# Kernel tuning notes

Measured on AMD Instinct MI355X. Metric: run time of the kernel, lower is better.

The kernel has to match this reference:

```python
import jax, jax.numpy as jnp
import numpy as np

B, S, D = 4, 256, 2048
E, F, K = 32, 768, 8


def setup_inputs() -> dict:
    key = jax.random.key(0)
    k1, k2, k3, k4, k5 = jax.random.split(key, 5)
    sc_in = 1.0 / np.sqrt(D)
    sc_f = 1.0 / np.sqrt(F)
    return {
        "hidden_states": jax.random.normal(k1, (B, S, D), jnp.float32),
        "gate_w": jax.random.normal(k2, (E, D), jnp.float32) * sc_in,   # nn.Linear(D, E).weight
        "wg": jax.random.normal(k3, (E, F, D), jnp.float32) * sc_in,    # gate_proj weights [E, F, D]
        "wu": jax.random.normal(k4, (E, F, D), jnp.float32) * sc_in,    # up_proj weights   [E, F, D]
        "wd": jax.random.normal(k5, (E, D, F), jnp.float32) * sc_f,     # down_proj weights [E, D, F]
    }


def reference(hidden_states, gate_w, wg, wu, wd):
    b, s, d = hidden_states.shape
    x = hidden_states.reshape(-1, d)                        # [T, D]
    T = x.shape[0]

    # Router: linear -> softmax over experts -> top-k -> renormalize
    router_logits = jnp.einsum("td,ed->te", x, gate_w)      # [T, E]
    routing_probs = jax.nn.softmax(router_logits, axis=-1)
    topk_w, topk_idx = jax.lax.top_k(routing_probs, K)      # [T, K]
    topk_w = topk_w / jnp.sum(topk_w, axis=-1, keepdims=True)  # norm_topk_prob=True

    # Scatter top-k weights to dense [T, E] combine weights (zeros for unselected experts)
    combine = jnp.zeros((T, wg.shape[0]), x.dtype).at[
        jnp.arange(T)[:, None], topk_idx
    ].set(topk_w)                                           # [T, E]

    # Expert gated MLPs (computed for all experts, combined with sparse weights)
    g = jnp.einsum("td,efd->etf", x, wg)                    # [E, T, F]
    u = jnp.einsum("td,efd->etf", x, wu)                    # [E, T, F]
    h = jax.nn.silu(g) * u                                  # [E, T, F]
    y = jnp.einsum("etf,edf->etd", h, wd)                   # [E, T, D]

    out = jnp.einsum("te,etd->td", combine, y)              # [T, D]
    return out.reshape(b, s, d)
```

## Files before the change

### kernel.cpp

```cpp
#include <hip/hip_runtime.h>

#define T_TOK 1024
#define D_DIM 2048
#define E_NUM 32
#define F_DIM 768
#define K_TOP 8

typedef __bf16 v8bf __attribute__((ext_vector_type(8)));
typedef float v4f __attribute__((ext_vector_type(4)));
typedef unsigned short v8us __attribute__((ext_vector_type(8)));

__device__ __forceinline__ unsigned short f2b(float f) {
  unsigned int u = __builtin_bit_cast(unsigned int, f);
  u += 0x7fffu + ((u >> 16) & 1u);
  return (unsigned short)(u >> 16);
}
__device__ __forceinline__ float b2f(unsigned short s) {
  return __builtin_bit_cast(float, (unsigned int)s << 16);
}
__device__ __forceinline__ v8us cvt8u(v4f a, v4f b) {
  v8bf r;
  r[0] = (__bf16)a[0]; r[1] = (__bf16)a[1]; r[2] = (__bf16)a[2]; r[3] = (__bf16)a[3];
  r[4] = (__bf16)b[0]; r[5] = (__bf16)b[1]; r[6] = (__bf16)b[2]; r[7] = (__bf16)b[3];
  return __builtin_bit_cast(v8us, r);
}
__device__ __forceinline__ void gload16(const void* g, void* l) {
  __builtin_amdgcn_global_load_lds(
      (const __attribute__((address_space(1))) void*)g,
      (__attribute__((address_space(3))) void*)l, 16, 0, 0);
}
__device__ __forceinline__ v4f gload4f(const char* p) {
  v4f r;
  asm volatile("global_load_dwordx4 %0, %1, off" : "=v"(r) : "v"(p));
  return r;
}

#define VMWAIT(N) asm volatile("s_waitcnt vmcnt(" #N ")" ::: "memory")
#define LGKM0() asm volatile("s_waitcnt lgkmcnt(0)" ::: "memory")
#define SBAR() __builtin_amdgcn_s_barrier()
#define SCHEDB() __builtin_amdgcn_sched_barrier(0)

__global__ __launch_bounds__(256) void router_kernel(
    const float* __restrict__ x, const float* __restrict__ gw,
    unsigned short* __restrict__ xb, int* __restrict__ counts,
    int* __restrict__ tlist, int* __restrict__ topk_e, int* __restrict__ topk_p,
    float* __restrict__ topk_w, float* __restrict__ wlist)
{
  const int t = blockIdx.x, tid = threadIdx.x;
  const float* xr = x + (size_t)t * D_DIM;

  {
    v4f f0 = *reinterpret_cast<const v4f*>(xr + tid * 8);
    v4f f1 = *reinterpret_cast<const v4f*>(xr + tid * 8 + 4);
    *reinterpret_cast<v8us*>(xb + (size_t)t * D_DIM + tid * 8) = cvt8u(f0, f1);
  }

  __shared__ float logits[E_NUM];
  const int lane = tid & 63, wave = tid >> 6;
  for (int j = 0; j < 8; ++j) {
    int e = wave * 8 + j;
    const float* wr = gw + (size_t)e * D_DIM;
    float s = 0.f;
#pragma unroll
    for (int i = 0; i < D_DIM / 64; ++i) s = fmaf(xr[lane + i * 64], wr[lane + i * 64], s);
#pragma unroll
    for (int off = 32; off > 0; off >>= 1) s += __shfl_xor(s, off);
    if (lane == 0) logits[e] = s;
  }
  __syncthreads();

  if (tid == 0) {
    float lg[E_NUM];
#pragma unroll
    for (int e2 = 0; e2 < E_NUM; ++e2) lg[e2] = logits[e2];
    int sel[K_TOP]; float sv[K_TOP];
    for (int k = 0; k < K_TOP; ++k) {
      int best = 0; float bv = -3.4e38f;
      for (int e2 = 0; e2 < E_NUM; ++e2)
        if (lg[e2] > bv) { bv = lg[e2]; best = e2; }
      sel[k] = best; sv[k] = bv; lg[best] = -3.4e38f;
    }
    float mx = sv[0], s8 = 0.f, ww[K_TOP];
    for (int k = 0; k < K_TOP; ++k) { ww[k] = __expf(sv[k] - mx); s8 += ww[k]; }
    float inv = 1.f / s8;
    for (int k = 0; k < K_TOP; ++k) {
      float w = ww[k] * inv;
      int e2 = sel[k];
      int pos = atomicAdd(&counts[e2], 1);
      tlist[e2 * T_TOK + pos] = t;
      wlist[e2 * T_TOK + pos] = w;
      topk_e[t * K_TOP + k] = e2;
      topk_p[t * K_TOP + k] = pos;
      topk_w[t * K_TOP + k] = w;
    }
  }
}

__global__ void scan_kernel(const int* __restrict__ counts, int* __restrict__ offsets)
{
  if (threadIdx.x == 0) {
    int run = 0;
    for (int e = 0; e < E_NUM; ++e) { offsets[e] = run; run += counts[e]; }
  }
}

__global__ __launch_bounds__(512, 4) void gateup_kernel(
    const unsigned short* __restrict__ xb, const float* __restrict__ wg,
    const float* __restrict__ wu, const int* __restrict__ counts,
    const int* __restrict__ offsets, const int* __restrict__ tlist,
    unsigned short* __restrict__ hbuf)
{
  const int e = blockIdx.y;
  const int cnt = counts[e];
  const int tf = blockIdx.x % 12;
  const int tm = blockIdx.x / 12;
  if (tm * 192 >= cnt) return;

  __shared__ __align__(16) unsigned char lds[81920];

  const int tid = threadIdx.x;
  const int lane = tid & 63;
  const int wave = tid >> 6;
  const int wm = wave >> 1;
  const int wn = wave & 1;
  const int l15 = lane & 15;
  const int l4 = lane >> 4;

  const char* xbB = (const char*)xb;
  unsigned asrc[3], adst[3];
#pragma unroll
  for (int c = 0; c < 3; ++c) {
    int idx = tid + c * 512;
    int r = idx >> 3, gl = idx & 7;
    int rg = tm * 192 + r;
    if (rg > cnt - 1) rg = cnt - 1;
    int tok = tlist[e * T_TOK + rg];
    int gg = gl ^ (r & 7);
    asrc[c] = (unsigned)tok * 4096u + (unsigned)(gg * 16);
    adst[c] = (unsigned)(idx * 16);
  }
  const int brow = tid >> 3, bg8 = tid & 7;
  const unsigned bsrc = (unsigned)((tf * 64 + brow) * 8192 + bg8 * 32);
  const unsigned bdst = (unsigned)(brow * 128 + ((bg8 ^ (brow & 7)) * 16));
  const char* gB = (const char*)wg + (size_t)e * F_DIM * D_DIM * 4;
  const char* uB = (const char*)wu + (size_t)e * F_DIM * D_DIM * 4;

  unsigned aRd[3];
#pragma unroll
  for (int fm = 0; fm < 3; ++fm) {
    int row = wm * 48 + fm * 16 + l15;
    aRd[fm] = (unsigned)(row * 128 + ((l4 ^ (row & 7)) * 16));
  }
  unsigned bRd[2];
#pragma unroll
  for (int fn = 0; fn < 2; ++fn) {
    int row = wn * 32 + fn * 16 + l15;
    bRd[fn] = (unsigned)(row * 128 + ((l4 ^ (row & 7)) * 16));
  }

  v4f zero = {0.f, 0.f, 0.f, 0.f};
  v4f accg[3][2], accu[3][2];
#pragma unroll
  for (int fm = 0; fm < 3; ++fm)
#pragma unroll
    for (int fn = 0; fn < 2; ++fn) { accg[fm][fn] = zero; accu[fm][fn] = zero; }

  auto COMPUTE = [&](unsigned ab, unsigned bb, unsigned sx) {
    v8bf af[3], bg[2], bu[2];
#pragma unroll
    for (int fm = 0; fm < 3; ++fm)
      af[fm] = __builtin_bit_cast(v8bf,
          *reinterpret_cast<const v8us*>(&lds[ab + (aRd[fm] ^ sx)]));
#pragma unroll
    for (int fn = 0; fn < 2; ++fn) {
      bg[fn] = __builtin_bit_cast(v8bf,
          *reinterpret_cast<const v8us*>(&lds[bb + (bRd[fn] ^ sx)]));
      bu[fn] = __builtin_bit_cast(v8bf,
          *reinterpret_cast<const v8us*>(&lds[bb + 8192u + (bRd[fn] ^ sx)]));
    }
#pragma unroll
    for (int fm = 0; fm < 3; ++fm)
#pragma unroll
      for (int fn = 0; fn < 2; ++fn) {
        accg[fm][fn] = __builtin_amdgcn_mfma_f32_16x16x32_bf16(af[fm], bg[fn], accg[fm][fn], 0, 0, 0);
        accu[fm][fn] = __builtin_amdgcn_mfma_f32_16x16x32_bf16(af[fm], bu[fn], accu[fm][fn], 0, 0, 0);
      }
  };

  const int NG = D_DIM / 64;

  v4f g0 = gload4f(gB + bsrc);
  v4f g1 = gload4f(gB + bsrc + 16);
  v4f u0 = gload4f(uB + bsrc);
  v4f u1 = gload4f(uB + bsrc + 16);
  SCHEDB();
#pragma unroll
  for (int c = 0; c < 3; ++c) gload16(xbB + asrc[c], &lds[adst[c]]);
  SCHEDB();

#pragma unroll 2
  for (int i = 0; i < NG; ++i) {
    const unsigned ab = (unsigned)(i & 1) * 24576u;
    const unsigned bb = 49152u + (unsigned)(i & 1) * 16384u;
    VMWAIT(3); SCHEDB();
    *reinterpret_cast<v8us*>(&lds[bb + bdst]) = cvt8u(g0, g1);
    *reinterpret_cast<v8us*>(&lds[bb + 8192u + bdst]) = cvt8u(u0, u1);
    if (i + 1 < NG) {
      const unsigned an = (unsigned)((i + 1) & 1) * 24576u;
      unsigned bo = bsrc + (unsigned)(i + 1) * 256u;
      g0 = gload4f(gB + bo);
      g1 = gload4f(gB + bo + 16);
      u0 = gload4f(uB + bo);
      u1 = gload4f(uB + bo + 16);
      SCHEDB();
      unsigned ao = (unsigned)(i + 1) * 128u;
#pragma unroll
      for (int c = 0; c < 3; ++c) gload16(xbB + asrc[c] + ao, &lds[an + adst[c]]);
      SCHEDB();
      VMWAIT(7);
    } else {
      VMWAIT(0);
    }
    SCHEDB(); LGKM0(); SBAR(); SCHEDB();
    COMPUTE(ab, bb, 0u);
    COMPUTE(ab, bb, 64u);
    SCHEDB(); SBAR();
  }

  const int off_e = offsets[e];
#pragma unroll
  for (int fm = 0; fm < 3; ++fm)
#pragma unroll
    for (int fn = 0; fn < 2; ++fn)
#pragma unroll
      for (int i = 0; i < 4; ++i) {
        int rloc = wm * 48 + fm * 16 + l4 * 4 + i;
        int rg = tm * 192 + rloc;
        if (rg < cnt) {
          int col = tf * 64 + wn * 32 + fn * 16 + l15;
          float g = accg[fm][fn][i];
          float uu = accu[fm][fn][i];
          float h = g * (1.f / (1.f + __expf(-g))) * uu;
          hbuf[(size_t)(off_e + rg) * F_DIM + col] = f2b(h);
        }
      }
}

template <int STAGEOUT>
__global__ __launch_bounds__(512, 4) void down_kernel(
    const unsigned short* __restrict__ hbuf, const float* __restrict__ wd,
    const int* __restrict__ counts, const int* __restrict__ offsets,
    const int* __restrict__ tlist, const float* __restrict__ wlist,
    unsigned short* __restrict__ ybuf, float* __restrict__ out)
{
  const int e = blockIdx.y;
  const int cnt = counts[e];
  const int td = blockIdx.x % 32;
  const int tm = blockIdx.x / 32;
  if (tm * 192 >= cnt) return;
  const int off_e = offsets[e];

  __shared__ __align__(16) unsigned char lds[65536];

  const int tid = threadIdx.x;
  const int lane = tid & 63;
  const int wave = tid >> 6;
  const int wm = wave >> 1;
  const int wn = wave & 1;
  const int l15 = lane & 15;
  const int l4 = lane >> 4;

  const char* hB = (const char*)hbuf;
  unsigned asrc[3], adst[3];
#pragma unroll
  for (int c = 0; c < 3; ++c) {
    int idx = tid + c * 512;
    int r = idx >> 3, gl = idx & 7;
    int rg = tm * 192 + r;
    if (rg > cnt - 1) rg = cnt - 1;
    int gg = gl ^ (r & 7);
    asrc[c] = (unsigned)(off_e + rg) * 1536u + (unsigned)(gg * 16);
    adst[c] = (unsigned)(idx * 16);
  }
  const int brow = tid >> 3, bg8 = tid & 7;
  const unsigned bsrc = (unsigned)((td * 64 + brow) * 3072 + bg8 * 32);
  const unsigned bdst = (unsigned)(brow * 128 + ((bg8 ^ (brow & 7)) * 16));
  const char* bB = (const char*)wd + (size_t)e * D_DIM * F_DIM * 4;

  unsigned aRd[3];
#pragma unroll
  for (int fm = 0; fm < 3; ++fm) {
    int row = wm * 48 + fm * 16 + l15;
    aRd[fm] = (unsigned)(row * 128 + ((l4 ^ (row & 7)) * 16));
  }
  unsigned bRd[2];
#pragma unroll
  for (int fn = 0; fn < 2; ++fn) {
    int row = wn * 32 + fn * 16 + l15;
    bRd[fn] = (unsigned)(row * 128 + ((l4 ^ (row & 7)) * 16));
  }

  v4f zero = {0.f, 0.f, 0.f, 0.f};
  v4f acc[3][2];
#pragma unroll
  for (int fm = 0; fm < 3; ++fm)
#pragma unroll
    for (int fn = 0; fn < 2; ++fn) acc[fm][fn] = zero;

  auto COMPUTE = [&](unsigned ab, unsigned bb, unsigned sx) {
    v8bf af[3], bf_[2];
#pragma unroll
    for (int fm = 0; fm < 3; ++fm)
      af[fm] = __builtin_bit_cast(v8bf,
          *reinterpret_cast<const v8us*>(&lds[ab + (aRd[fm] ^ sx)]));
#pragma unroll
    for (int fn = 0; fn < 2; ++fn)
      bf_[fn] = __builtin_bit_cast(v8bf,
          *reinterpret_cast<const v8us*>(&lds[bb + (bRd[fn] ^ sx)]));
#pragma unroll
    for (int fm = 0; fm < 3; ++fm)
#pragma unroll
      for (int fn = 0; fn < 2; ++fn)
        acc[fm][fn] = __builtin_amdgcn_mfma_f32_16x16x32_bf16(af[fm], bf_[fn], acc[fm][fn], 0, 0, 0);
  };

  const int NG = F_DIM / 64;

  v4f b0 = gload4f(bB + bsrc);
  v4f b1 = gload4f(bB + bsrc + 16);
  SCHEDB();
#pragma unroll
  for (int c = 0; c < 3; ++c) gload16(hB + asrc[c], &lds[adst[c]]);
  SCHEDB();

#pragma unroll 2
  for (int i = 0; i < NG; ++i) {
    const unsigned ab = (unsigned)(i & 1) * 24576u;
    const unsigned bb = 49152u + (unsigned)(i & 1) * 8192u;
    VMWAIT(3); SCHEDB();
    *reinterpret_cast<v8us*>(&lds[bb + bdst]) = cvt8u(b0, b1);
    if (i + 1 < NG) {
      const unsigned an = (unsigned)((i + 1) & 1) * 24576u;
      unsigned bo = bsrc + (unsigned)(i + 1) * 256u;
      b0 = gload4f(bB + bo);
      b1 = gload4f(bB + bo + 16);
      SCHEDB();
      unsigned ao = (unsigned)(i + 1) * 128u;
#pragma unroll
      for (int c = 0; c < 3; ++c) gload16(hB + asrc[c] + ao, &lds[an + adst[c]]);
      SCHEDB();
      VMWAIT(5);
    } else {
      VMWAIT(0);
    }
    SCHEDB(); LGKM0(); SBAR(); SCHEDB();
    COMPUTE(ab, bb, 0u);
    COMPUTE(ab, bb, 64u);
    SCHEDB(); SBAR();
  }

#pragma unroll
  for (int fm = 0; fm < 3; ++fm)
#pragma unroll
    for (int fn = 0; fn < 2; ++fn)
#pragma unroll
      for (int i = 0; i < 4; ++i) {
        int rloc = wm * 48 + fm * 16 + l4 * 4 + i;
        int rg = tm * 192 + rloc;
        if (rg < cnt) {
          int col = td * 64 + wn * 32 + fn * 16 + l15;
          float y = acc[fm][fn][i];
          if (STAGEOUT) {
            ybuf[(size_t)(off_e + rg) * D_DIM + col] = f2b(y);
          } else {
            int tok = tlist[e * T_TOK + rg];
            float w = wlist[e * T_TOK + rg];
            atomicAdd(out + (size_t)tok * D_DIM + col, w * y);
          }
        }
      }
}

__global__ __launch_bounds__(256) void combine_kernel(
    const unsigned short* __restrict__ ybuf, const int* __restrict__ topk_e,
    const int* __restrict__ topk_p, const float* __restrict__ topk_w,
    const int* __restrict__ offsets, float* __restrict__ out)
{
  const int t = blockIdx.x, tid = threadIdx.x;
  const int d0 = tid * 8;
  float acc[8] = {0.f, 0.f, 0.f, 0.f, 0.f, 0.f, 0.f, 0.f};
#pragma unroll
  for (int k = 0; k < K_TOP; ++k) {
    int e = topk_e[t * K_TOP + k];
    int slot = offsets[e] + topk_p[t * K_TOP + k];
    float w = topk_w[t * K_TOP + k];
    v8us v = *reinterpret_cast<const v8us*>(ybuf + (size_t)slot * D_DIM + d0);
#pragma unroll
    for (int j = 0; j < 8; ++j) acc[j] += w * b2f(v[j]);
  }
  v4f o0 = {acc[0], acc[1], acc[2], acc[3]};
  v4f o1 = {acc[4], acc[5], acc[6], acc[7]};
  *reinterpret_cast<v4f*>(out + (size_t)t * D_DIM + d0) = o0;
  *reinterpret_cast<v4f*>(out + (size_t)t * D_DIM + d0 + 4) = o1;
}

extern "C" void kernel_launch(void* const* d_in, const int* in_sizes, int n_in,
                              void* d_out, int out_size, void* d_ws, size_t ws_size,
                              hipStream_t stream)
{
  const float* x  = (const float*)d_in[0];
  const float* gw = (const float*)d_in[1];
  const float* wg = (const float*)d_in[2];
  const float* wu = (const float*)d_in[3];
  const float* wd = (const float*)d_in[4];
  float* out = (float*)d_out;

  char* p = (char*)d_ws;
  auto alloc = [&](size_t bytes) {
    char* r = p;
    p += (bytes + 255) & ~(size_t)255;
    return r;
  };
  int* counts   = (int*)alloc(E_NUM * 4);
  int* offsets  = (int*)alloc(E_NUM * 4);
  int* tlist    = (int*)alloc((size_t)E_NUM * T_TOK * 4);
  float* wlist  = (float*)alloc((size_t)E_NUM * T_TOK * 4);
  int* topk_e   = (int*)alloc((size_t)T_TOK * K_TOP * 4);
  int* topk_p   = (int*)alloc((size_t)T_TOK * K_TOP * 4);
  float* topk_w = (float*)alloc((size_t)T_TOK * K_TOP * 4);
  unsigned short* xb   = (unsigned short*)alloc((size_t)T_TOK * D_DIM * 2);
  unsigned short* hbuf = (unsigned short*)alloc((size_t)T_TOK * K_TOP * F_DIM * 2);
  size_t need_atomic = (size_t)(p - (char*)d_ws);
  unsigned short* ybuf = (unsigned short*)alloc((size_t)T_TOK * K_TOP * D_DIM * 2);
  size_t need_stage = (size_t)(p - (char*)d_ws);

  if (ws_size < need_atomic) return;
  const bool stage = (ws_size >= need_stage);

  hipMemsetAsync(counts, 0, E_NUM * 4, stream);
  router_kernel<<<T_TOK, 256, 0, stream>>>(x, gw, xb, counts, tlist, topk_e, topk_p, topk_w, wlist);
  scan_kernel<<<1, 64, 0, stream>>>(counts, offsets);
  gateup_kernel<<<dim3(12 * 2, E_NUM), 512, 0, stream>>>(
      xb, wg, wu, counts, offsets, tlist, hbuf);
  if (stage) {
    down_kernel<1><<<dim3(32 * 2, E_NUM), 512, 0, stream>>>(
        hbuf, wd, counts, offsets, tlist, wlist, ybuf, out);
    combine_kernel<<<T_TOK, 256, 0, stream>>>(ybuf, topk_e, topk_p, topk_w, offsets, out);
  } else {
    hipMemsetAsync(out, 0, (size_t)out_size * 4, stream);
    down_kernel<0><<<dim3(32 * 2, E_NUM), 512, 0, stream>>>(
        hbuf, wd, counts, offsets, tlist, wlist, ybuf, out);
  }
}
```

Before: 298.0 us.

## Cover both token tiles per block in MoE GEMMs so weights load once

The gate/up and down expert GEMM kernels now have each block compute both 192-row token tiles of an expert, instead of launching one block per token tile. This removes the duplicate fp32 weight streaming and bf16 conversion that happened whenever an expert had more than 192 tokens. The N tiles also grow: 96 columns for gate/up and 128 for down. LDS use and accumulator count rise, launch bounds drop to one block per CU, and the grids shrink. The trade is less occupancy and fewer blocks for less global weight traffic.

```diff
diff --git a/kernel.cpp b/kernel.cpp
--- a/kernel.cpp
+++ b/kernel.cpp
@@ -104,7 +104,7 @@
   }
 }
 
-__global__ __launch_bounds__(512, 4) void gateup_kernel(
+__global__ __launch_bounds__(512, 1) void gateup_kernel(
     const unsigned short* __restrict__ xb, const float* __restrict__ wg,
     const float* __restrict__ wu, const int* __restrict__ counts,
     const int* __restrict__ offsets, const int* __restrict__ tlist,
@@ -112,11 +112,10 @@
 {
   const int e = blockIdx.y;
   const int cnt = counts[e];
-  const int tf = blockIdx.x % 12;
-  const int tm = blockIdx.x / 12;
-  if (tm * 192 >= cnt) return;
-
-  __shared__ __align__(16) unsigned char lds[81920];
+  const int tf = blockIdx.x;
+  const bool two = cnt > 192;
+
+  __shared__ __align__(16) unsigned char lds[147456];
 
   const int tid = threadIdx.x;
   const int lane = tid & 63;
@@ -127,23 +126,34 @@
   const int l4 = lane >> 4;
 
   const char* xbB = (const char*)xb;
-  unsigned asrc[3], adst[3];
+  const int gl = tid & 7;
+  unsigned asrc[6];
+#pragma unroll
+  for (int c = 0; c < 6; ++c) {
+    int rp = (tid >> 3) + c * 64;
+    int row = rp % 192;
+    int tm = rp / 192;
+    int rg = tm * 192 + row;
+    if (rg > cnt - 1) rg = cnt - 1;
+    int tok = tlist[e * T_TOK + rg];
+    int gg = gl ^ (row & 7);
+    asrc[c] = (unsigned)tok * 4096u + (unsigned)(gg * 16);
+  }
+  const unsigned adst0 = (unsigned)(tid * 16);
+
+  const char* gB = (const char*)wg + (size_t)e * F_DIM * D_DIM * 4;
+  const char* uB = (const char*)wu + (size_t)e * F_DIM * D_DIM * 4;
+  const char* bp[3];
+  unsigned bdst[3];
 #pragma unroll
   for (int c = 0; c < 3; ++c) {
     int idx = tid + c * 512;
-    int r = idx >> 3, gl = idx & 7;
-    int rg = tm * 192 + r;
-    if (rg > cnt - 1) rg = cnt - 1;
-    int tok = tlist[e * T_TOK + rg];
-    int gg = gl ^ (r & 7);
-    asrc[c] = (unsigned)tok * 4096u + (unsigned)(gg * 16);
-    adst[c] = (unsigned)(idx * 16);
-  }
-  const int brow = tid >> 3, bg8 = tid & 7;
-  const unsigned bsrc = (unsigned)((tf * 64 + brow) * 8192 + bg8 * 32);
-  const unsigned bdst = (unsigned)(brow * 128 + ((bg8 ^ (brow & 7)) * 16));
-  const char* gB = (const char*)wg + (size_t)e * F_DIM * D_DIM * 4;
-  const char* uB = (const char*)wu + (size_t)e * F_DIM * D_DIM * 4;
+    int mat = idx >= 768;
+    int mi = mat ? idx - 768 : idx;
+    int row = mi >> 3, pr = mi & 7;
+    bp[c] = (mat ? uB : gB) + (size_t)(tf * 96 + row) * 8192 + pr * 32;
+    bdst[c] = (unsigned)(mat * 12288 + row * 128 + ((pr ^ (row & 7)) * 16));
+  }
 
   unsigned aRd[3];
 #pragma unroll
@@ -151,103 +161,109 @@
     int row = wm * 48 + fm * 16 + l15;
     aRd[fm] = (unsigned)(row * 128 + ((l4 ^ (row & 7)) * 16));
   }
-  unsigned bRd[2];
-#pragma unroll
-  for (int fn = 0; fn < 2; ++fn) {
-    int row = wn * 32 + fn * 16 + l15;
+  unsigned bRd[3];
+#pragma unroll
+  for (int fn = 0; fn < 3; ++fn) {
+    int row = wn * 48 + fn * 16 + l15;
     bRd[fn] = (unsigned)(row * 128 + ((l4 ^ (row & 7)) * 16));
   }
 
   v4f zero = {0.f, 0.f, 0.f, 0.f};
-  v4f accg[3][2], accu[3][2];
-#pragma unroll
-  for (int fm = 0; fm < 3; ++fm)
-#pragma unroll
-    for (int fn = 0; fn < 2; ++fn) { accg[fm][fn] = zero; accu[fm][fn] = zero; }
-
-  auto COMPUTE = [&](unsigned ab, unsigned bb, unsigned sx) {
-    v8bf af[3], bg[2], bu[2];
+  v4f accg[2][3][3], accu[2][3][3];
+#pragma unroll
+  for (int tm = 0; tm < 2; ++tm)
+#pragma unroll
+    for (int fm = 0; fm < 3; ++fm)
+#pragma unroll
+      for (int fn = 0; fn < 3; ++fn) { accg[tm][fm][fn] = zero; accu[tm][fm][fn] = zero; }
+
+  auto COMPUTE = [&](int tm, unsigned ab, unsigned bb, unsigned sx) {
+    v8bf af[3], bg[3], bu[3];
+    const unsigned at = ab + (unsigned)tm * 24576u;
 #pragma unroll
     for (int fm = 0; fm < 3; ++fm)
       af[fm] = __builtin_bit_cast(v8bf,
-          *reinterpret_cast<const v8us*>(&lds[ab + (aRd[fm] ^ sx)]));
-#pragma unroll
-    for (int fn = 0; fn < 2; ++fn) {
+          *reinterpret_cast<const v8us*>(&lds[at + (aRd[fm] ^ sx)]));
+#pragma unroll
+    for (int fn = 0; fn < 3; ++fn) {
       bg[fn] = __builtin_bit_cast(v8bf,
           *reinterpret_cast<const v8us*>(&lds[bb + (bRd[fn] ^ sx)]));
       bu[fn] = __builtin_bit_cast(v8bf,
-          *reinterpret_cast<const v8us*>(&lds[bb + 8192u + (bRd[fn] ^ sx)]));
-    }
-#pragma unroll
-    for (int fm = 0; fm < 3; ++fm)
-#pragma unroll
-      for (int fn = 0; fn < 2; ++fn) {
-        accg[fm][fn] = __builtin_amdgcn_mfma_f32_16x16x32_bf16(af[fm], bg[fn], accg[fm][fn], 0, 0, 0);
-        accu[fm][fn] = __builtin_amdgcn_mfma_f32_16x16x32_bf16(af[fm], bu[fn], accu[fm][fn], 0, 0, 0);
+          *reinterpret_cast<const v8us*>(&lds[bb + 12288u + (bRd[fn] ^ sx)]));
+    }
+#pragma unroll
+    for (int fm = 0; fm < 3; ++fm)
+#pragma unroll
+      for (int fn = 0; fn < 3; ++fn) {
+        accg[tm][fm][fn] = __builtin_amdgcn_mfma_f32_16x16x32_bf16(af[fm], bg[fn], accg[tm][fm][fn], 0, 0, 0);
+        accu[tm][fm][fn] = __builtin_amdgcn_mfma_f32_16x16x32_bf16(af[fm], bu[fn], accu[tm][fm][fn], 0, 0, 0);
       }
   };
 
   const int NG = D_DIM / 64;
 
-  v4f g0 = gload4f(gB + bsrc);
-  v4f g1 = gload4f(gB + bsrc + 16);
-  v4f u0 = gload4f(uB + bsrc);
-  v4f u1 = gload4f(uB + bsrc + 16);
+  v4f b0[3], b1[3];
+#pragma unroll
+  for (int c = 0; c < 3; ++c) { b0[c] = gload4f(bp[c]); b1[c] = gload4f(bp[c] + 16); }
   SCHEDB();
 #pragma unroll
-  for (int c = 0; c < 3; ++c) gload16(xbB + asrc[c], &lds[adst[c]]);
+  for (int c = 0; c < 6; ++c) gload16(xbB + asrc[c], &lds[adst0 + c * 8192u]);
   SCHEDB();
 
 #pragma unroll 2
   for (int i = 0; i < NG; ++i) {
-    const unsigned ab = (unsigned)(i & 1) * 24576u;
-    const unsigned bb = 49152u + (unsigned)(i & 1) * 16384u;
-    VMWAIT(3); SCHEDB();
-    *reinterpret_cast<v8us*>(&lds[bb + bdst]) = cvt8u(g0, g1);
-    *reinterpret_cast<v8us*>(&lds[bb + 8192u + bdst]) = cvt8u(u0, u1);
+    const unsigned ab = (unsigned)(i & 1) * 49152u;
+    const unsigned bb = 98304u + (unsigned)(i & 1) * 24576u;
+    VMWAIT(6); SCHEDB();
+#pragma unroll
+    for (int c = 0; c < 3; ++c)
+      *reinterpret_cast<v8us*>(&lds[bb + bdst[c]]) = cvt8u(b0[c], b1[c]);
     if (i + 1 < NG) {
-      const unsigned an = (unsigned)((i + 1) & 1) * 24576u;
-      unsigned bo = bsrc + (unsigned)(i + 1) * 256u;
-      g0 = gload4f(gB + bo);
-      g1 = gload4f(gB + bo + 16);
-      u0 = gload4f(uB + bo);
-      u1 = gload4f(uB + bo + 16);
+      const unsigned an = (unsigned)((i + 1) & 1) * 49152u;
+      const unsigned ko = (unsigned)(i + 1) * 256u;
+#pragma unroll
+      for (int c = 0; c < 3; ++c) { b0[c] = gload4f(bp[c] + ko); b1[c] = gload4f(bp[c] + ko + 16); }
       SCHEDB();
-      unsigned ao = (unsigned)(i + 1) * 128u;
-#pragma unroll
-      for (int c = 0; c < 3; ++c) gload16(xbB + asrc[c] + ao, &lds[an + adst[c]]);
+      const unsigned ao = (unsigned)(i + 1) * 128u;
+#pragma unroll
+      for (int c = 0; c < 6; ++c) gload16(xbB + asrc[c] + ao, &lds[an + adst0 + c * 8192u]);
       SCHEDB();
-      VMWAIT(7);
+      VMWAIT(12);
     } else {
       VMWAIT(0);
     }
     SCHEDB(); LGKM0(); SBAR(); SCHEDB();
-    COMPUTE(ab, bb, 0u);
-    COMPUTE(ab, bb, 64u);
+    COMPUTE(0, ab, bb, 0u);
+    COMPUTE(0, ab, bb, 64u);
+    if (two) {
+      COMPUTE(1, ab, bb, 0u);
+      COMPUTE(1, ab, bb, 64u);
+    }
     SCHEDB(); SBAR();
   }
 
   const int off_e = offsets[e];
 #pragma unroll
-  for (int fm = 0; fm < 3; ++fm)
-#pragma unroll
-    for (int fn = 0; fn < 2; ++fn)
-#pragma unroll
-      for (int i = 0; i < 4; ++i) {
-        int rloc = wm * 48 + fm * 16 + l4 * 4 + i;
-        int rg = tm * 192 + rloc;
-        if (rg < cnt) {
-          int col = tf * 64 + wn * 32 + fn * 16 + l15;
-          float g = accg[fm][fn][i];
-          float uu = accu[fm][fn][i];
-          float h = g * (1.f / (1.f + __expf(-g))) * uu;
-          hbuf[(size_t)(off_e + rg) * F_DIM + col] = f2b(h);
+  for (int tm = 0; tm < 2; ++tm)
+#pragma unroll
+    for (int fm = 0; fm < 3; ++fm)
+#pragma unroll
+      for (int fn = 0; fn < 3; ++fn)
+#pragma unroll
+        for (int i = 0; i < 4; ++i) {
+          int rg = tm * 192 + wm * 48 + fm * 16 + l4 * 4 + i;
+          if (rg < cnt) {
+            int col = tf * 96 + wn * 48 + fn * 16 + l15;
+            float g = accg[tm][fm][fn][i];
+            float uu = accu[tm][fm][fn][i];
+            float h = g * (1.f / (1.f + __expf(-g))) * uu;
+            hbuf[(size_t)(off_e + rg) * F_DIM + col] = f2b(h);
+          }
         }
-      }
 }
 
 template <int STAGEOUT>
-__global__ __launch_bounds__(512, 4) void down_kernel(
+__global__ __launch_bounds__(512, 1) void down_kernel(
     const unsigned short* __restrict__ hbuf, const float* __restrict__ wd,
     const int* __restrict__ counts, const int* __restrict__ offsets,
     const int* __restrict__ tlist, const float* __restrict__ wlist,
@@ -255,12 +271,11 @@
 {
   const int e = blockIdx.y;
   const int cnt = counts[e];
-  const int td = blockIdx.x % 32;
-  const int tm = blockIdx.x / 32;
-  if (tm * 192 >= cnt) return;
+  const int td = blockIdx.x;
+  const bool two = cnt > 192;
   const int off_e = offsets[e];
 
-  __shared__ __align__(16) unsigned char lds[65536];
+  __shared__ __align__(16) unsigned char lds[131072];
 
   const int tid = threadIdx.x;
   const int lane = tid & 63;
@@ -271,21 +286,30 @@
   const int l4 = lane >> 4;
 
   const char* hB = (const char*)hbuf;
-  unsigned asrc[3], adst[3];
-#pragma unroll
-  for (int c = 0; c < 3; ++c) {
+  const int gl = tid & 7;
+  unsigned asrc[6];
+#pragma unroll
+  for (int c = 0; c < 6; ++c) {
+    int rp = (tid >> 3) + c * 64;
+    int row = rp % 192;
+    int tm = rp / 192;
+    int rg = tm * 192 + row;
+    if (rg > cnt - 1) rg = cnt - 1;
+    int gg = gl ^ (row & 7);
+    asrc[c] = (unsigned)(off_e + rg) * 1536u + (unsigned)(gg * 16);
+  }
+  const unsigned adst0 = (unsigned)(tid * 16);
+
+  const char* bB = (const char*)wd + (size_t)e * D_DIM * F_DIM * 4;
+  const char* bp[2];
+  unsigned bdst[2];
+#pragma unroll
+  for (int c = 0; c < 2; ++c) {
     int idx = tid + c * 512;
-    int r = idx >> 3, gl = idx & 7;
-    int rg = tm * 192 + r;
-    if (rg > cnt - 1) rg = cnt - 1;
-    int gg = gl ^ (r & 7);
-    asrc[c] = (unsigned)(off_e + rg) * 1536u + (unsigned)(gg * 16);
-    adst[c] = (unsigned)(idx * 16);
-  }
-  const int brow = tid >> 3, bg8 = tid & 7;
-  const unsigned bsrc = (unsigned)((td * 64 + brow) * 3072 + bg8 * 32);
-  const unsigned bdst = (unsigned)(brow * 128 + ((bg8 ^ (brow & 7)) * 16));
-  const char* bB = (const char*)wd + (size_t)e * D_DIM * F_DIM * 4;
+    int row = idx >> 3, pr = idx & 7;
+    bp[c] = bB + (size_t)(td * 128 + row) * 3072 + pr * 32;
+    bdst[c] = (unsigned)(row * 128 + ((pr ^ (row & 7)) * 16));
+  }
 
   unsigned aRd[3];
 #pragma unroll
@@ -293,92 +317,103 @@
     int row = wm * 48 + fm * 16 + l15;
     aRd[fm] = (unsigned)(row * 128 + ((l4 ^ (row & 7)) * 16));
   }
-  unsigned bRd[2];
-#pragma unroll
-  for (int fn = 0; fn < 2; ++fn) {
-    int row = wn * 32 + fn * 16 + l15;
+  unsigned bRd[4];
+#pragma unroll
+  for (int fn = 0; fn < 4; ++fn) {
+    int row = wn * 64 + fn * 16 + l15;
     bRd[fn] = (unsigned)(row * 128 + ((l4 ^ (row & 7)) * 16));
   }
 
   v4f zero = {0.f, 0.f, 0.f, 0.f};
-  v4f acc[3][2];
-#pragma unroll
-  for (int fm = 0; fm < 3; ++fm)
-#pragma unroll
-    for (int fn = 0; fn < 2; ++fn) acc[fm][fn] = zero;
-
-  auto COMPUTE = [&](unsigned ab, unsigned bb, unsigned sx) {
-    v8bf af[3], bf_[2];
+  v4f acc[2][3][4];
+#pragma unroll
+  for (int tm = 0; tm < 2; ++tm)
+#pragma unroll
+    for (int fm = 0; fm < 3; ++fm)
+#pragma unroll
+      for (int fn = 0; fn < 4; ++fn) acc[tm][fm][fn] = zero;
+
+  auto COMPUTE = [&](int tm, unsigned ab, unsigned bb, unsigned sx) {
+    v8bf af[3], bf_[4];
+    const unsigned at = ab + (unsigned)tm * 24576u;
 #pragma unroll
     for (int fm = 0; fm < 3; ++fm)
       af[fm] = __builtin_bit_cast(v8bf,
-          *reinterpret_cast<const v8us*>(&lds[ab + (aRd[fm] ^ sx)]));
-#pragma unroll
-    for (int fn = 0; fn < 2; ++fn)
+          *reinterpret_cast<const v8us*>(&lds[at + (aRd[fm] ^ sx)]));
+#pragma unroll
+    for (int fn = 0; fn < 4; ++fn)
       bf_[fn] = __builtin_bit_cast(v8bf,
           *reinterpret_cast<const v8us*>(&lds[bb + (bRd[fn] ^ sx)]));
 #pragma unroll
     for (int fm = 0; fm < 3; ++fm)
 #pragma unroll
-      for (int fn = 0; fn < 2; ++fn)
-        acc[fm][fn] = __builtin_amdgcn_mfma_f32_16x16x32_bf16(af[fm], bf_[fn], acc[fm][fn], 0, 0, 0);
+      for (int fn = 0; fn < 4; ++fn)
+        acc[tm][fm][fn] = __builtin_amdgcn_mfma_f32_16x16x32_bf16(af[fm], bf_[fn], acc[tm][fm][fn], 0, 0, 0);
   };
 
   const int NG = F_DIM / 64;
 
-  v4f b0 = gload4f(bB + bsrc);
-  v4f b1 = gload4f(bB + bsrc + 16);
+  v4f b0[2], b1[2];
+#pragma unroll
+  for (int c = 0; c < 2; ++c) { b0[c] = gload4f(bp[c]); b1[c] = gload4f(bp[c] + 16); }
   SCHEDB();
 #pragma unroll
-  for (int c = 0; c < 3; ++c) gload16(hB + asrc[c], &lds[adst[c]]);
+  for (int c = 0; c < 6; ++c) gload16(hB + asrc[c], &lds[adst0 + c * 8192u]);
   SCHEDB();
 
 #pragma unroll 2
   for (int i = 0; i < NG; ++i) {
-    const unsigned ab = (unsigned)(i & 1) * 24576u;
-    const unsigned bb = 49152u + (unsigned)(i & 1) * 8192u;
-    VMWAIT(3); SCHEDB();
-    *reinterpret_cast<v8us*>(&lds[bb + bdst]) = cvt8u(b0, b1);
+    const unsigned ab = (unsigned)(i & 1) * 49152u;
+    const unsigned bb = 98304u + (unsigned)(i & 1) * 16384u;
+    VMWAIT(6); SCHEDB();
+#pragma unroll
+    for (int c = 0; c < 2; ++c)
+      *reinterpret_cast<v8us*>(&lds[bb + bdst[c]]) = cvt8u(b0[c], b1[c]);
     if (i + 1 < NG) {
-      const unsigned an = (unsigned)((i + 1) & 1) * 24576u;
-      unsigned bo = bsrc + (unsigned)(i + 1) * 256u;
-      b0 = gload4f(bB + bo);
-      b1 = gload4f(bB + bo + 16);
+      const unsigned an = (unsigned)((i + 1) & 1) * 49152u;
+      const unsigned ko = (unsigned)(i + 1) * 256u;
+#pragma unroll
+      for (int c = 0; c < 2; ++c) { b0[c] = gload4f(bp[c] + ko); b1[c] = gload4f(bp[c] + ko + 16); }
       SCHEDB();
-      unsigned ao = (unsigned)(i + 1) * 128u;
-#pragma unroll
-      for (int c = 0; c < 3; ++c) gload16(hB + asrc[c] + ao, &lds[an + adst[c]]);
+      const unsigned ao = (unsigned)(i + 1) * 128u;
+#pragma unroll
+      for (int c = 0; c < 6; ++c) gload16(hB + asrc[c] + ao, &lds[an + adst0 + c * 8192u]);
       SCHEDB();
-      VMWAIT(5);
+      VMWAIT(10);
     } else {
       VMWAIT(0);
     }
     SCHEDB(); LGKM0(); SBAR(); SCHEDB();
-    COMPUTE(ab, bb, 0u);
-    COMPUTE(ab, bb, 64u);
+    COMPUTE(0, ab, bb, 0u);
+    COMPUTE(0, ab, bb, 64u);
+    if (two) {
+      COMPUTE(1, ab, bb, 0u);
+      COMPUTE(1, ab, bb, 64u);
+    }
     SCHEDB(); SBAR();
   }
 
 #pragma unroll
-  for (int fm = 0; fm < 3; ++fm)
-#pragma unroll
-    for (int fn = 0; fn < 2; ++fn)
-#pragma unroll
-      for (int i = 0; i < 4; ++i) {
-        int rloc = wm * 48 + fm * 16 + l4 * 4 + i;
-        int rg = tm * 192 + rloc;
-        if (rg < cnt) {
-          int col = td * 64 + wn * 32 + fn * 16 + l15;
-          float y = acc[fm][fn][i];
-          if (STAGEOUT) {
-            ybuf[(size_t)(off_e + rg) * D_DIM + col] = f2b(y);
-          } else {
-            int tok = tlist[e * T_TOK + rg];
-            float w = wlist[e * T_TOK + rg];
-            atomicAdd(out + (size_t)tok * D_DIM + col, w * y);
+  for (int tm = 0; tm < 2; ++tm)
+#pragma unroll
+    for (int fm = 0; fm < 3; ++fm)
+#pragma unroll
+      for (int fn = 0; fn < 4; ++fn)
+#pragma unroll
+        for (int i = 0; i < 4; ++i) {
+          int rg = tm * 192 + wm * 48 + fm * 16 + l4 * 4 + i;
+          if (rg < cnt) {
+            int col = td * 128 + wn * 64 + fn * 16 + l15;
+            float y = acc[tm][fm][fn][i];
+            if (STAGEOUT) {
+              ybuf[(size_t)(off_e + rg) * D_DIM + col] = f2b(y);
+            } else {
+              int tok = tlist[e * T_TOK + rg];
+              float w = wlist[e * T_TOK + rg];
+              atomicAdd(out + (size_t)tok * D_DIM + col, w * y);
+            }
           }
         }
-      }
 }
 
 __global__ __launch_bounds__(256) void combine_kernel(
@@ -440,15 +475,15 @@
   hipMemsetAsync(counts, 0, E_NUM * 4, stream);
   router_kernel<<<T_TOK, 256, 0, stream>>>(x, gw, xb, counts, tlist, topk_e, topk_p, topk_w, wlist);
   scan_kernel<<<1, 64, 0, stream>>>(counts, offsets);
-  gateup_kernel<<<dim3(12 * 2, E_NUM), 512, 0, stream>>>(
+  gateup_kernel<<<dim3(8, E_NUM), 512, 0, stream>>>(
       xb, wg, wu, counts, offsets, tlist, hbuf);
   if (stage) {
-    down_kernel<1><<<dim3(32 * 2, E_NUM), 512, 0, stream>>>(
+    down_kernel<1><<<dim3(16, E_NUM), 512, 0, stream>>>(
         hbuf, wd, counts, offsets, tlist, wlist, ybuf, out);
     combine_kernel<<<T_TOK, 256, 0, stream>>>(ybuf, topk_e, topk_p, topk_w, offsets, out);
   } else {
     hipMemsetAsync(out, 0, (size_t)out_size * 4, stream);
-    down_kernel<0><<<dim3(32 * 2, E_NUM), 512, 0, stream>>>(
+    down_kernel<0><<<dim3(16, E_NUM), 512, 0, stream>>>(
         hbuf, wd, counts, offsets, tlist, wlist, ybuf, out);
   }
 }
```

New measurement: 526.6 us. 76.7% more time.
